# Kernel optimization log

Measured on AMD Instinct MI355X. Metric: run time of the kernel, lower is better.

## Reference

```python
import jax, jax.numpy as jnp
import numpy as np

T = 8192
C = 768
HEAD = 64

def setup_inputs() -> dict:
    key = jax.random.key(0)
    k0, k1, k2, k3 = jax.random.split(key, 4)
    tokens = jax.random.normal(k0, (T, C), dtype=jnp.float32)
    Wk = jax.random.normal(k1, (C, HEAD), dtype=jnp.float32) * (1.0 / np.sqrt(C))
    Wq = jax.random.normal(k2, (C, HEAD), dtype=jnp.float32) * (1.0 / np.sqrt(C))
    Wv = jax.random.normal(k3, (C, HEAD), dtype=jnp.float32) * (1.0 / np.sqrt(C))
    return {"tokens": tokens, "Wk": Wk, "Wq": Wq, "Wv": Wv}

def reference(tokens, Wk, Wq, Wv):
    # Single-head causal attention, faithful to source (scale = C**0.5, a multiply).
    keys = tokens @ Wk          # [T, H]
    queries = tokens @ Wq       # [T, H]
    values = tokens @ Wv        # [T, H]
    c = tokens.shape[-1]
    wei = (queries @ keys.T) * (c ** 0.5)                 # [T, T]
    causal = jnp.tril(jnp.ones((tokens.shape[0], tokens.shape[0]), dtype=bool))
    wei = jnp.where(causal, wei, -jnp.inf)
    wei = jax.nn.softmax(wei, axis=-1)
    return wei @ values         # [T, H]; dropout inactive (training=False)
```

## Files before the change

kernel.cpp:

```cpp
#include <hip/hip_runtime.h>
#include <math.h>

#define T_TOK 8192
#define C_DIM 768
#define H_DIM 64
#define SCALE_LOG2E (27.712812921102035f * 1.4426950408889634f)
#define NSPLIT 4

typedef _Float16 half8 __attribute__((ext_vector_type(8)));
typedef _Float16 half2t __attribute__((ext_vector_type(2)));
typedef float floatx4 __attribute__((ext_vector_type(4)));

#define MFMA16(a, b, c) __builtin_amdgcn_mfma_f32_16x16x32_f16(a, b, c, 0, 0, 0)
#define WAIT_LGKM0() __builtin_amdgcn_s_waitcnt(0xC07F)
#define EXP2F(x) __builtin_amdgcn_exp2f(x)

typedef __attribute__((address_space(3))) void lds_void;
typedef const __attribute__((address_space(1))) void gbl_void;
#define GLOAD16(gp, lp) \
    __builtin_amdgcn_global_load_lds((gbl_void*)(gp), (lds_void*)(lp), 16, 0, 0)

template <int K> struct IC { static constexpr int v = K; };


__global__ __launch_bounds__(64) void wconvert_kernel(
    const float* __restrict__ Wk, const float* __restrict__ Wq,
    const float* __restrict__ Wv, _Float16* __restrict__ WF)
{
    const int b = blockIdx.x;
    const int mat = b / 96, rem = b % 96, kt = rem >> 2, nb = rem & 3;
    const int lane = threadIdx.x & 63, l15 = lane & 15, quad = lane >> 4;
    const float* __restrict__ W = (mat == 0) ? Wk : (mat == 1) ? Wq : Wv;

    half8 h, l;
#pragma unroll
    for (int j = 0; j < 8; ++j) {
        const float v = W[(kt * 32 + quad * 8 + j) * H_DIM + nb * 16 + l15];
        const _Float16 hv = (_Float16)v;
        h[j] = hv;
        l[j] = (_Float16)(v - (float)hv);
    }
    _Float16* dst = WF + ((((size_t)mat * 24 + kt) * 4 + nb) * 2) * 512 + lane * 8;
    *(half8*)dst = h;
    *(half8*)(dst + 512) = l;
}

__global__ __launch_bounds__(128, 1) void proj_kernel(
    const float* __restrict__ tokens, const _Float16* __restrict__ WF,
    _Float16* __restrict__ KF, _Float16* __restrict__ QF,
    _Float16* __restrict__ VF)
{
    __shared__ __align__(16) char smemraw[81920];
    const int b = blockIdx.x;
    const int tid = threadIdx.x;
    const int w = tid >> 6;
    const int lane = tid & 63, l15 = lane & 15, quad = lane >> 4;
    const int row0 = b * 32;
    const int kt0 = w * 12;

    floatx4 acc[3][2][4];
#pragma unroll
    for (int mat = 0; mat < 3; ++mat)
#pragma unroll
        for (int mb = 0; mb < 2; ++mb)
#pragma unroll
            for (int nb = 0; nb < 4; ++nb) acc[mat][mb][nb] = 0;

    const float* __restrict__ xb0 =
        tokens + (size_t)(row0 + l15) * C_DIM + kt0 * 32 + quad * 8;
    const float* __restrict__ xb1 =
        tokens + (size_t)(row0 + 16 + l15) * C_DIM + kt0 * 32 + quad * 8;

    _Float16* const wavebuf = (_Float16*)(smemraw + w * 40960);


    {
#pragma unroll
        for (int nb = 0; nb < 4; ++nb) {
            const _Float16* gK =
                WF + (size_t)((kt0 * 4 + nb) * 2) * 512 + lane * 8;
            const _Float16* gQ =
                WF + (size_t)(((24 + kt0) * 4 + nb) * 2) * 512 + lane * 8;
            const _Float16* gV =
                WF + (size_t)(((48 + kt0) * 4 + nb) * 2) * 512 + lane * 8;
            GLOAD16(gK,       wavebuf + (nb * 2 + 0) * 512);
            GLOAD16(gK + 512, wavebuf + (nb * 2 + 1) * 512);
            GLOAD16(gQ,       wavebuf + (8 + nb * 2 + 0) * 512);
            GLOAD16(gQ + 512, wavebuf + (8 + nb * 2 + 1) * 512);
            GLOAD16(gV,       wavebuf + (16 + nb) * 512);
        }
    }
    __builtin_amdgcn_sched_barrier(0);
    float4 tf[4][4];
#pragma unroll
    for (int d = 0; d < 4; ++d) {
        tf[d][0] = *(const float4*)(xb0 + d * 32);
        tf[d][1] = *(const float4*)(xb0 + d * 32 + 4);
        tf[d][2] = *(const float4*)(xb1 + d * 32);
        tf[d][3] = *(const float4*)(xb1 + d * 32 + 4);
    }
    __builtin_amdgcn_sched_barrier(0);

    auto iter = [&](auto kc) {
        constexpr int ktl = decltype(kc)::v;
        constexpr int slot = ktl & 3;
        constexpr int curb = ktl & 1;
        _Float16* wb  = wavebuf + curb * 10240;
        _Float16* wbn = wavebuf + (curb ^ 1) * 10240;

        __builtin_amdgcn_sched_barrier(0);
        const float4 x0 = tf[slot][0], x1 = tf[slot][1];
        const float4 x2 = tf[slot][2], x3 = tf[slot][3];
        __builtin_amdgcn_sched_barrier(0);

        if constexpr (ktl < 11) {
            const int ktn = kt0 + ktl + 1;
#pragma unroll
            for (int nb = 0; nb < 4; ++nb) {
                const _Float16* gK =
                    WF + (size_t)((ktn * 4 + nb) * 2) * 512 + lane * 8;
                const _Float16* gQ =
                    WF + (size_t)(((24 + ktn) * 4 + nb) * 2) * 512 + lane * 8;
                const _Float16* gV =
                    WF + (size_t)(((48 + ktn) * 4 + nb) * 2) * 512 + lane * 8;
                GLOAD16(gK,       wbn + (nb * 2 + 0) * 512);
                GLOAD16(gK + 512, wbn + (nb * 2 + 1) * 512);
                GLOAD16(gQ,       wbn + (8 + nb * 2 + 0) * 512);
                GLOAD16(gQ + 512, wbn + (8 + nb * 2 + 1) * 512);
                GLOAD16(gV,       wbn + (16 + nb) * 512);
            }
        }
        __builtin_amdgcn_sched_barrier(0);
        if constexpr (ktl + 4 < 12) {
            constexpr int ktf = ktl + 4;
            tf[slot][0] = *(const float4*)(xb0 + ktf * 32);
            tf[slot][1] = *(const float4*)(xb0 + ktf * 32 + 4);
            tf[slot][2] = *(const float4*)(xb1 + ktf * 32);
            tf[slot][3] = *(const float4*)(xb1 + ktf * 32 + 4);
        }
        __builtin_amdgcn_sched_barrier(0);
        constexpr int VMN = (ktl == 0)
            ? 40
            : ((ktl <= 8 ? 4 : 0) + (ktl <= 10 ? 20 : 0) + (ktl <= 7 ? 4 : 0));
        asm volatile("s_waitcnt vmcnt(%0)" ::"n"(VMN));
        __builtin_amdgcn_sched_barrier(0);

        half8 ah[2], al[2];
        {
            const float xs0[8] = {x0.x, x0.y, x0.z, x0.w, x1.x, x1.y, x1.z, x1.w};
            const float xs1[8] = {x2.x, x2.y, x2.z, x2.w, x3.x, x3.y, x3.z, x3.w};
#pragma unroll
            for (int e = 0; e < 8; ++e) {
                _Float16 hv = (_Float16)xs0[e];
                ah[0][e] = hv;
                al[0][e] = (_Float16)(xs0[e] - (float)hv);
                hv = (_Float16)xs1[e];
                ah[1][e] = hv;
                al[1][e] = (_Float16)(xs1[e] - (float)hv);
            }
        }
        const _Float16* wp = wb + lane * 8;
#pragma unroll
        for (int nb = 0; nb < 4; ++nb) {
            const half8 kh = *(const half8*)(wp + (nb * 2 + 0) * 512);
            const half8 kl = *(const half8*)(wp + (nb * 2 + 1) * 512);
            const half8 qh = *(const half8*)(wp + (8 + nb * 2 + 0) * 512);
            const half8 ql = *(const half8*)(wp + (8 + nb * 2 + 1) * 512);
            const half8 vh = *(const half8*)(wp + (16 + nb) * 512);
#pragma unroll
            for (int mb = 0; mb < 2; ++mb) {
                acc[0][mb][nb] = MFMA16(ah[mb], kh, acc[0][mb][nb]);
                acc[0][mb][nb] = MFMA16(ah[mb], kl, acc[0][mb][nb]);
                acc[0][mb][nb] = MFMA16(al[mb], kh, acc[0][mb][nb]);
                acc[1][mb][nb] = MFMA16(ah[mb], qh, acc[1][mb][nb]);
                acc[1][mb][nb] = MFMA16(ah[mb], ql, acc[1][mb][nb]);
                acc[1][mb][nb] = MFMA16(al[mb], qh, acc[1][mb][nb]);
                acc[2][mb][nb] = MFMA16(ah[mb], vh, acc[2][mb][nb]);
            }
        }
    };
#define PITER(k) iter(IC<k>{});
    PITER(0)  PITER(1)  PITER(2)  PITER(3)  PITER(4)  PITER(5)
    PITER(6)  PITER(7)  PITER(8)  PITER(9)  PITER(10) PITER(11)
#undef PITER

    __syncthreads();

    float* Cb0 = (float*)smemraw;
    float* Cb1 = (float*)(smemraw + 26112);
    float* Cbw = w ? Cb1 : Cb0;
#pragma unroll
    for (int mat = 0; mat < 3; ++mat)
#pragma unroll
        for (int mb = 0; mb < 2; ++mb)
#pragma unroll
            for (int nb = 0; nb < 4; ++nb)
#pragma unroll
                for (int r = 0; r < 4; ++r)
                    Cbw[mat * 2176 + (mb * 16 + quad * 4 + r) * 68 + nb * 16 + l15] =
                        acc[mat][mb][nb][r];
    __syncthreads();

    {
        const int nbL = w;
#pragma unroll
        for (int ks = 0; ks < 2; ++ks) {
            {
                const int off = (nbL * 16 + l15) * 68 + ks * 32 + quad * 8;
                const float4 a0 = *(const float4*)(Cb0 + off);
                const float4 a1 = *(const float4*)(Cb0 + off + 4);
                const float4 b0 = *(const float4*)(Cb1 + off);
                const float4 b1 = *(const float4*)(Cb1 + off + 4);
                const float cs[8] = {a0.x + b0.x, a0.y + b0.y, a0.z + b0.z,
                                     a0.w + b0.w, a1.x + b1.x, a1.y + b1.y,
                                     a1.z + b1.z, a1.w + b1.w};
                half8 h, l;
#pragma unroll
                for (int e = 0; e < 8; ++e) {
                    const _Float16 hv = (_Float16)cs[e];
                    h[e] = hv;
                    l[e] = (_Float16)(cs[e] - (float)hv);
                }
                const int t = b >> 1, nb = (b & 1) * 2 + nbL;
                _Float16* dst =
                    KF + (((size_t)(t * 4 + nb) * 2 + ks) * 2) * 512 + lane * 8;
                *(half8*)dst = h;
                *(half8*)(dst + 512) = l;
            }
            {
                const int off =
                    2176 + (nbL * 16 + l15) * 68 + ks * 32 + quad * 8;
                const float4 a0 = *(const float4*)(Cb0 + off);
                const float4 a1 = *(const float4*)(Cb0 + off + 4);
                const float4 b0 = *(const float4*)(Cb1 + off);
                const float4 b1 = *(const float4*)(Cb1 + off + 4);
                const float cs[8] = {a0.x + b0.x, a0.y + b0.y, a0.z + b0.z,
                                     a0.w + b0.w, a1.x + b1.x, a1.y + b1.y,
                                     a1.z + b1.z, a1.w + b1.w};
                half8 h, l;
#pragma unroll
                for (int e = 0; e < 8; ++e) {
                    const _Float16 hv = (_Float16)cs[e];
                    h[e] = hv;
                    l[e] = (_Float16)(cs[e] - (float)hv);
                }
                const int rb = b * 2 + nbL;
                _Float16* dst = QF + (((size_t)rb * 2 + ks) * 2) * 512 + lane * 8;
                *(half8*)dst = h;
                *(half8*)(dst + 512) = l;
            }
        }
    }

    {
        const int t = b >> 1, ks = b & 1;
#pragma unroll
        for (int nbi = 0; nbi < 2; ++nbi) {
            const int nb = w * 2 + nbi;
            half8 h;
#pragma unroll
            for (int j = 0; j < 8; ++j) {
                const int off = 2 * 2176 + (quad * 8 + j) * 68 + nb * 16 + l15;
                h[j] = (_Float16)(Cb0[off] + Cb1[off]);
            }
            *(half8*)(VF + ((size_t)(t * 4 + nb) * 2 + ks) * 512 + lane * 8) = h;
        }
    }
}

__global__ __launch_bounds__(512, 2) void attn_mfma_kernel(
    const _Float16* __restrict__ QF, const _Float16* __restrict__ KF,
    const _Float16* __restrict__ VF,
    float* __restrict__ pm, float* __restrict__ pl, float* __restrict__ po)
{
    __shared__ __align__(16) float smemf[9984];
    _Float16* Ps = (_Float16*)smemf;
    float* aL = smemf + 9216;
    float* mP = smemf + 9472;
    float* lP = smemf + 9728;

    const int w = threadIdx.x >> 6, lane = threadIdx.x & 63;
    const int l15 = lane & 15, quad = lane >> 4;
    const int mhalf = w & 1, ss = w >> 1;

    const int b = blockIdx.x;
    const int j = b & 255, hb = b >> 8;
    const int qt = (hb == 0) ? (j >> 1) : (127 - (j >> 1));
    const int sp = (hb << 1) | (j & 1);

    const int qbase = qt * 64;
    const int wrow0 = qbase + mhalf * 32;

    half8 qh[2][2], ql[2][2];
#pragma unroll
    for (int mb = 0; mb < 2; ++mb)
#pragma unroll
        for (int ks = 0; ks < 2; ++ks) {
            const int rb = qt * 4 + mhalf * 2 + mb;
            const _Float16* qp = QF + (((size_t)rb * 2 + ks) * 2) * 512 + lane * 8;
            qh[mb][ks] = *(const half8*)qp;
            ql[mb][ks] = *(const half8*)(qp + 512);
        }

    floatx4 O[2][4];
#pragma unroll
    for (int mb = 0; mb < 2; ++mb)
#pragma unroll
        for (int nb = 0; nb < 4; ++nb) O[mb][nb] = 0;
    float mq[2] = {-INFINITY, -INFINITY};
    float lq[2] = {0.f, 0.f};

    const int t0 = sp + 4 * ss;
    half8 kh[4][2], kl[4][2];
    if (t0 <= qt) {
#pragma unroll
        for (int kb2 = 0; kb2 < 4; ++kb2)
#pragma unroll
            for (int ks = 0; ks < 2; ++ks) {
                const _Float16* kp =
                    KF + (((size_t)(t0 * 4 + kb2) * 2 + ks) * 2) * 512 + lane * 8;
                kh[kb2][ks] = *(const half8*)kp;
                kl[kb2][ks] = *(const half8*)(kp + 512);
            }
    }

    for (int t = t0; t <= qt; t += 16) {
        const int kb = t * 64;

        half8 v0r[4], v1r[4];
#pragma unroll
        for (int nb = 0; nb < 4; ++nb) {
            const _Float16* vp = VF + ((size_t)(t * 4 + nb) * 2) * 512 + lane * 8;
            v0r[nb] = *(const half8*)vp;
            v1r[nb] = *(const half8*)(vp + 512);
        }

        float sv[4][2][4];
#pragma unroll
        for (int kb2 = 0; kb2 < 4; ++kb2)
#pragma unroll
            for (int qb = 0; qb < 2; ++qb) {
                floatx4 s = 0;
#pragma unroll
                for (int ks = 0; ks < 2; ++ks) {
                    s = MFMA16(kh[kb2][ks], qh[qb][ks], s);
                    s = MFMA16(kl[kb2][ks], qh[qb][ks], s);
                    s = MFMA16(kh[kb2][ks], ql[qb][ks], s);
                }
#pragma unroll
                for (int r = 0; r < 4; ++r) sv[kb2][qb][r] = s[r] * SCALE_LOG2E;
            }

        if (t + 16 <= qt) {
            const int tn = t + 16;
#pragma unroll
            for (int kb2 = 0; kb2 < 4; ++kb2)
#pragma unroll
                for (int ks = 0; ks < 2; ++ks) {
                    const _Float16* kp =
                        KF + (((size_t)(tn * 4 + kb2) * 2 + ks) * 2) * 512 + lane * 8;
                    kh[kb2][ks] = *(const half8*)kp;
                    kl[kb2][ks] = *(const half8*)(kp + 512);
                }
        }

        if (kb + 63 > wrow0) {
#pragma unroll
            for (int qb = 0; qb < 2; ++qb) {
                const int q = wrow0 + qb * 16 + l15;
#pragma unroll
                for (int kb2 = 0; kb2 < 4; ++kb2) {
                    const int keyb = kb + kb2 * 16 + quad * 4;
#pragma unroll
                    for (int r = 0; r < 4; ++r)
                        if (keyb + r > q) sv[kb2][qb][r] = -INFINITY;
                }
            }
        }

#pragma unroll
        for (int qb = 0; qb < 2; ++qb) {
            float rm = sv[0][qb][0];
#pragma unroll
            for (int kb2 = 0; kb2 < 4; ++kb2)
#pragma unroll
                for (int r = 0; r < 4; ++r) rm = fmaxf(rm, sv[kb2][qb][r]);
            rm = fmaxf(rm, __shfl_xor(rm, 16));
            rm = fmaxf(rm, __shfl_xor(rm, 32));
            const float mnew = fmaxf(mq[qb], rm);
            const float alpha = EXP2F(mq[qb] - mnew);
            if (quad == 0) aL[w * 32 + qb * 16 + l15] = alpha;
            float psum = 0.f;
#pragma unroll
            for (int kb2 = 0; kb2 < 4; ++kb2) {
                const float p0 = EXP2F(sv[kb2][qb][0] - mnew);
                const float p1 = EXP2F(sv[kb2][qb][1] - mnew);
                const float p2 = EXP2F(sv[kb2][qb][2] - mnew);
                const float p3 = EXP2F(sv[kb2][qb][3] - mnew);
                psum += (p0 + p1) + (p2 + p3);
                const unsigned u0 =
                    __builtin_bit_cast(unsigned, __builtin_amdgcn_cvt_pkrtz(p0, p1));
                const unsigned u1 =
                    __builtin_bit_cast(unsigned, __builtin_amdgcn_cvt_pkrtz(p2, p3));
                uint2* dst = (uint2*)(Ps + (w * 2 + qb) * 1152 + l15 * 72 +
                                      kb2 * 16 + quad * 4);
                *dst = make_uint2(u0, u1);
            }
            lq[qb] = lq[qb] * alpha + psum;
            mq[qb] = mnew;
        }

        __builtin_amdgcn_wave_barrier();
        WAIT_LGKM0();
        __builtin_amdgcn_wave_barrier();

        floatx4 aO[2];
#pragma unroll
        for (int mb = 0; mb < 2; ++mb)
            aO[mb] = *(const floatx4*)(aL + w * 32 + mb * 16 + quad * 4);
#pragma unroll
        for (int mb = 0; mb < 2; ++mb)
#pragma unroll
            for (int nb = 0; nb < 4; ++nb)
#pragma unroll
                for (int r = 0; r < 4; ++r) O[mb][nb][r] *= aO[mb][r];

        half8 pa0[2], pa1[2];
#pragma unroll
        for (int mb = 0; mb < 2; ++mb) {
            const _Float16* pp = Ps + (w * 2 + mb) * 1152 + l15 * 72 + quad * 8;
            pa0[mb] = *(const half8*)pp;
            pa1[mb] = *(const half8*)(pp + 32);
        }

#pragma unroll
        for (int nb = 0; nb < 4; ++nb) {
#pragma unroll
            for (int mb = 0; mb < 2; ++mb) {
                O[mb][nb] = MFMA16(pa0[mb], v0r[nb], O[mb][nb]);
                O[mb][nb] = MFMA16(pa1[mb], v1r[nb], O[mb][nb]);
            }
        }
        __builtin_amdgcn_wave_barrier();
    }

#pragma unroll
    for (int qb = 0; qb < 2; ++qb) {
        lq[qb] += __shfl_xor(lq[qb], 16);
        lq[qb] += __shfl_xor(lq[qb], 32);
    }
    if (quad == 0) {
#pragma unroll
        for (int qb = 0; qb < 2; ++qb) {
            mP[w * 32 + qb * 16 + l15] = mq[qb];
            lP[w * 32 + qb * 16 + l15] = lq[qb];
        }
    }
    __builtin_amdgcn_wave_barrier();
    WAIT_LGKM0();
    __builtin_amdgcn_wave_barrier();
    float mreg[2][4], lreg[2][4];
#pragma unroll
    for (int mb = 0; mb < 2; ++mb) {
        const floatx4 mv = *(const floatx4*)(mP + w * 32 + mb * 16 + quad * 4);
        const floatx4 lv = *(const floatx4*)(lP + w * 32 + mb * 16 + quad * 4);
#pragma unroll
        for (int r = 0; r < 4; ++r) { mreg[mb][r] = mv[r]; lreg[mb][r] = lv[r]; }
    }

    __syncthreads();
    if (ss >= 2) {
        const int slot = ss - 2;
#pragma unroll
        for (int mb = 0; mb < 2; ++mb)
#pragma unroll
            for (int r = 0; r < 4; ++r) {
                const int row32 = mb * 16 + quad * 4 + r;
                const int sidx = (slot * 2 + mhalf) * 32 + row32;
#pragma unroll
                for (int nb = 0; nb < 4; ++nb)
                    smemf[sidx * 64 + nb * 16 + l15] = O[mb][nb][r];
                if (l15 == 0) {
                    smemf[8192 + sidx] = mreg[mb][r];
                    smemf[8320 + sidx] = lreg[mb][r];
                }
            }
    }
    __syncthreads();
    if (ss < 2) {
        const int slot = ss;
#pragma unroll
        for (int mb = 0; mb < 2; ++mb)
#pragma unroll
            for (int r = 0; r < 4; ++r) {
                const int row32 = mb * 16 + quad * 4 + r;
                const int sidx = (slot * 2 + mhalf) * 32 + row32;
                const float m1 = mreg[mb][r], l1 = lreg[mb][r];
                const float m2 = smemf[8192 + sidx];
                const float l2 = smemf[8320 + sidx];
                const float mm = fmaxf(m1, m2);
                const float a1 = (m1 == -INFINITY) ? 0.f : EXP2F(m1 - mm);
                const float a2 = (m2 == -INFINITY) ? 0.f : EXP2F(m2 - mm);
#pragma unroll
                for (int nb = 0; nb < 4; ++nb)
                    O[mb][nb][r] = O[mb][nb][r] * a1 +
                                   smemf[sidx * 64 + nb * 16 + l15] * a2;
                mreg[mb][r] = mm;
                lreg[mb][r] = l1 * a1 + l2 * a2;
            }
    }
    __syncthreads();
    if (ss == 1) {
#pragma unroll
        for (int mb = 0; mb < 2; ++mb)
#pragma unroll
            for (int r = 0; r < 4; ++r) {
                const int row32 = mb * 16 + quad * 4 + r;
                const int sidx = mhalf * 32 + row32;
#pragma unroll
                for (int nb = 0; nb < 4; ++nb)
                    smemf[sidx * 64 + nb * 16 + l15] = O[mb][nb][r];
                if (l15 == 0) {
                    smemf[8192 + sidx] = mreg[mb][r];
                    smemf[8320 + sidx] = lreg[mb][r];
                }
            }
    }
    __syncthreads();
    if (ss == 0) {
        const int pidx = qt * NSPLIT + sp;
#pragma unroll
        for (int mb = 0; mb < 2; ++mb)
#pragma unroll
            for (int r = 0; r < 4; ++r) {
                const int row32 = mb * 16 + quad * 4 + r;
                const int sidx = mhalf * 32 + row32;
                const float m1 = mreg[mb][r], l1 = lreg[mb][r];
                const float m2 = smemf[8192 + sidx];
                const float l2 = smemf[8320 + sidx];
                const float mm = fmaxf(m1, m2);
                const float a1 = (m1 == -INFINITY) ? 0.f : EXP2F(m1 - mm);
                const float a2 = (m2 == -INFINITY) ? 0.f : EXP2F(m2 - mm);
                const int row = mhalf * 32 + row32;
                float* dst = po + ((size_t)pidx * 64 + row) * 64;
#pragma unroll
                for (int nb = 0; nb < 4; ++nb)
                    dst[nb * 16 + l15] =
                        O[mb][nb][r] * a1 + smemf[sidx * 64 + nb * 16 + l15] * a2;
                if (l15 == 0) {
                    pm[pidx * 64 + row] = mm;
                    pl[pidx * 64 + row] = l1 * a1 + l2 * a2;
                }
            }
    }
}

__global__ __launch_bounds__(256) void combine_kernel(
    const float* __restrict__ pm, const float* __restrict__ pl,
    const float* __restrict__ po, float* __restrict__ out)
{
    const int vid = blockIdx.x * 256 + threadIdx.x;
    const int row = vid >> 4;
    const int d4  = vid & 15;
    const int qt  = row >> 6;
    const int r   = row & 63;

    float mm = -INFINITY;
#pragma unroll
    for (int s = 0; s < NSPLIT; ++s)
        mm = fmaxf(mm, pm[(qt * NSPLIT + s) * 64 + r]);
    float L = 0.f;
    float4 val = make_float4(0.f, 0.f, 0.f, 0.f);
#pragma unroll
    for (int s = 0; s < NSPLIT; ++s) {
        const int p = (qt * NSPLIT + s) * 64 + r;
        const float mp = pm[p];
        const float sc = (mp > -INFINITY) ? EXP2F(mp - mm) : 0.f;
        L += pl[p] * sc;
        const float4 v = *(const float4*)(po + (size_t)p * H_DIM + d4 * 4);
        val.x += v.x * sc; val.y += v.y * sc;
        val.z += v.z * sc; val.w += v.w * sc;
    }
    const float inv = 1.0f / L;
    float4 o; o.x = val.x * inv; o.y = val.y * inv;
    o.z = val.z * inv; o.w = val.w * inv;
    *(float4*)(out + (size_t)row * H_DIM + d4 * 4) = o;
}

extern "C" void kernel_launch(void* const* d_in, const int* in_sizes, int n_in,
                              void* d_out, int out_size, void* d_ws, size_t ws_size,
                              hipStream_t stream)
{
    const float* tokens = (const float*)d_in[0];
    const float* Wk = (const float*)d_in[1];
    const float* Wq = (const float*)d_in[2];
    const float* Wv = (const float*)d_in[3];
    float* out = (float*)d_out;

    char* ws = (char*)d_ws;
    const size_t MB = 1024 * 1024;
    _Float16* WF = (_Float16*)(ws + 0 * MB);
    _Float16* KF = (_Float16*)(ws + 1 * MB);
    _Float16* QF = (_Float16*)(ws + 3 * MB);
    _Float16* VF = (_Float16*)(ws + 5 * MB);
    float* pm = (float*)(ws + 6 * MB);
    float* pl = (float*)(ws + 6 * MB + 128 * 1024);
    float* po = (float*)(ws + 6 * MB + 256 * 1024);

    wconvert_kernel<<<288, 64, 0, stream>>>(Wk, Wq, Wv, WF);

    proj_kernel<<<256, 128, 0, stream>>>(tokens, WF, KF, QF, VF);

    attn_mfma_kernel<<<128 * NSPLIT, 512, 0, stream>>>(QF, KF, VF, pm, pl, po);

    combine_kernel<<<T_TOK * H_DIM / 4 / 256, 256, 0, stream>>>(pm, pl, po, out);
}
```

Before: 117.0 us.

## Defer online-softmax rescaling with threshold and raise priority around MFMA blocks

Adds a lazy-rescale path to the online softmax. When every row's new max stays within 8 (log2 units) of the running max across the wave, the alpha computation, the LDS round-trip and the rescale of the O accumulator are skipped. The scale multiply is folded into an fma inside the exp2. s_setprio is raised around both MFMA phases so that waves can interleave with other waves' softmax work. Deferred rescaling lets exponents grow up to 2^8 in the fp16 P values, which costs some precision headroom.

```diff
diff --git a/kernel.cpp b/kernel.cpp
--- a/kernel.cpp
+++ b/kernel.cpp
@@ -336,6 +336,7 @@
         }
 
         float sv[4][2][4];
+        __builtin_amdgcn_s_setprio(1);
 #pragma unroll
         for (int kb2 = 0; kb2 < 4; ++kb2)
 #pragma unroll
@@ -348,8 +349,9 @@
                     s = MFMA16(kh[kb2][ks], ql[qb][ks], s);
                 }
 #pragma unroll
-                for (int r = 0; r < 4; ++r) sv[kb2][qb][r] = s[r] * SCALE_LOG2E;
-            }
+                for (int r = 0; r < 4; ++r) sv[kb2][qb][r] = s[r];
+            }
+        __builtin_amdgcn_s_setprio(0);
 
         if (t + 16 <= qt) {
             const int tn = t + 16;
@@ -378,6 +380,7 @@
             }
         }
 
+        float rm_s[2];
 #pragma unroll
         for (int qb = 0; qb < 2; ++qb) {
             float rm = sv[0][qb][0];
@@ -387,16 +390,30 @@
                 for (int r = 0; r < 4; ++r) rm = fmaxf(rm, sv[kb2][qb][r]);
             rm = fmaxf(rm, __shfl_xor(rm, 16));
             rm = fmaxf(rm, __shfl_xor(rm, 32));
-            const float mnew = fmaxf(mq[qb], rm);
-            const float alpha = EXP2F(mq[qb] - mnew);
-            if (quad == 0) aL[w * 32 + qb * 16 + l15] = alpha;
+            rm_s[qb] = rm * SCALE_LOG2E;
+        }
+        const bool defer =
+            __all((rm_s[0] <= mq[0] + 8.f) && (rm_s[1] <= mq[1] + 8.f)) != 0;
+        if (!defer) {
+#pragma unroll
+            for (int qb = 0; qb < 2; ++qb) {
+                const float mnew = fmaxf(mq[qb], rm_s[qb]);
+                const float alpha = EXP2F(mq[qb] - mnew);
+                if (quad == 0) aL[w * 32 + qb * 16 + l15] = alpha;
+                lq[qb] *= alpha;
+                mq[qb] = mnew;
+            }
+        }
+#pragma unroll
+        for (int qb = 0; qb < 2; ++qb) {
+            const float nm = -mq[qb];
             float psum = 0.f;
 #pragma unroll
             for (int kb2 = 0; kb2 < 4; ++kb2) {
-                const float p0 = EXP2F(sv[kb2][qb][0] - mnew);
-                const float p1 = EXP2F(sv[kb2][qb][1] - mnew);
-                const float p2 = EXP2F(sv[kb2][qb][2] - mnew);
-                const float p3 = EXP2F(sv[kb2][qb][3] - mnew);
+                const float p0 = EXP2F(fmaf(sv[kb2][qb][0], SCALE_LOG2E, nm));
+                const float p1 = EXP2F(fmaf(sv[kb2][qb][1], SCALE_LOG2E, nm));
+                const float p2 = EXP2F(fmaf(sv[kb2][qb][2], SCALE_LOG2E, nm));
+                const float p3 = EXP2F(fmaf(sv[kb2][qb][3], SCALE_LOG2E, nm));
                 psum += (p0 + p1) + (p2 + p3);
                 const unsigned u0 =
                     __builtin_bit_cast(unsigned, __builtin_amdgcn_cvt_pkrtz(p0, p1));
@@ -406,24 +423,25 @@
                                       kb2 * 16 + quad * 4);
                 *dst = make_uint2(u0, u1);
             }
-            lq[qb] = lq[qb] * alpha + psum;
-            mq[qb] = mnew;
+            lq[qb] += psum;
         }
 
         __builtin_amdgcn_wave_barrier();
         WAIT_LGKM0();
         __builtin_amdgcn_wave_barrier();
 
-        floatx4 aO[2];
-#pragma unroll
-        for (int mb = 0; mb < 2; ++mb)
-            aO[mb] = *(const floatx4*)(aL + w * 32 + mb * 16 + quad * 4);
-#pragma unroll
-        for (int mb = 0; mb < 2; ++mb)
-#pragma unroll
-            for (int nb = 0; nb < 4; ++nb)
-#pragma unroll
-                for (int r = 0; r < 4; ++r) O[mb][nb][r] *= aO[mb][r];
+        if (!defer) {
+            floatx4 aO[2];
+#pragma unroll
+            for (int mb = 0; mb < 2; ++mb)
+                aO[mb] = *(const floatx4*)(aL + w * 32 + mb * 16 + quad * 4);
+#pragma unroll
+            for (int mb = 0; mb < 2; ++mb)
+#pragma unroll
+                for (int nb = 0; nb < 4; ++nb)
+#pragma unroll
+                    for (int r = 0; r < 4; ++r) O[mb][nb][r] *= aO[mb][r];
+        }
 
         half8 pa0[2], pa1[2];
 #pragma unroll
@@ -433,6 +451,7 @@
             pa1[mb] = *(const half8*)(pp + 32);
         }
 
+        __builtin_amdgcn_s_setprio(1);
 #pragma unroll
         for (int nb = 0; nb < 4; ++nb) {
 #pragma unroll
@@ -441,6 +460,7 @@
                 O[mb][nb] = MFMA16(pa1[mb], v1r[nb], O[mb][nb]);
             }
         }
+        __builtin_amdgcn_s_setprio(0);
         __builtin_amdgcn_wave_barrier();
     }
 
```

Result: no change. 118.3 us (+1.1%).
